# Performance work log

Measured on AMD Instinct MI355X. Metric: run time of the kernel, lower is better.

## Reference

```python
import jax, jax.numpy as jnp
import numpy as np
from jax import lax

HEADS = 8

def rotate_every_two(x):
    x1 = x[..., ::2]
    x2 = x[..., 1::2]
    return jnp.stack([-x2, x1], axis=-1).reshape(x.shape)

def theta_shift(x, sin, cos):
    # x: (b,n,N,d); sin/cos: (N,d) broadcast over b,n
    return x * cos + rotate_every_two(x) * sin

def setup_inputs() -> dict:
    key = jax.random.key(0)
    ks = jax.random.split(key, 8)
    B, C, H, W = 8, 256, 64, 64
    hd = C // HEADS
    return {
        'x': jax.random.normal(ks[0], (B, C, H, W), jnp.float32),
        'sin': jax.random.normal(ks[1], (H * W, hd), jnp.float32),
        'cos': jax.random.normal(ks[2], (H * W, hd), jnp.float32),
        'w_qkvo': jax.random.normal(ks[3], (4 * C, C), jnp.float32) * 0.02,
        'b_qkvo': jnp.zeros((4 * C,), jnp.float32),
        'w_lepe': jax.random.normal(ks[4], (C, 1, 5, 5), jnp.float32) * 0.02,
        'b_lepe': jnp.zeros((C,), jnp.float32),
        'w_proj': jax.random.normal(ks[5], (C, C), jnp.float32) * 0.02,
        'b_proj': jnp.zeros((C,), jnp.float32),
    }

def reference(x, sin, cos, w_qkvo, b_qkvo, w_lepe, b_lepe, w_proj, b_proj):
    B, C, H, W = x.shape
    heads = HEADS
    hd = C // heads
    N = H * W
    scale = hd ** (-0.5)

    # 1x1 conv qkvo
    qkvo = jnp.einsum('bchw,oc->bohw', x, w_qkvo) + b_qkvo[None, :, None, None]
    qkv = qkvo[:, :3 * C]
    o = qkvo[:, 3 * C:]

    # depthwise 5x5 lepe on v channels
    v_img = qkv[:, 2 * C:]
    lepe = lax.conv_general_dilated(
        v_img, w_lepe, (1, 1), [(2, 2), (2, 2)],
        dimension_numbers=('NCHW', 'OIHW', 'NCHW'),
        feature_group_count=C) + b_lepe[None, :, None, None]

    # b (m n d) h w -> m b n (h w) d
    qkv_r = qkv.reshape(B, 3, heads, hd, N).transpose(1, 0, 2, 4, 3)
    q, k, v = qkv_r[0], qkv_r[1], qkv_r[2]  # (b,n,N,d)

    q = jax.nn.elu(q) + 1.0
    k = jax.nn.elu(k) + 1.0

    # z = q @ mean_k^T * scale -> (b,n,N,1)
    z = jnp.einsum('bnld,bnd->bnl', q, k.mean(axis=2))[..., None] * scale

    q = theta_shift(q, sin, cos)
    k = theta_shift(k, sin, cos)

    s = (scale / N) ** 0.5
    kv = jnp.einsum('bnld,bnle->bnde', k * s, v * s)  # (b,n,d,d)
    v_mean = v.mean(axis=2, keepdims=True)  # (b,n,1,d)

    res = jnp.einsum('bnld,bnde->bnle', q, kv) * (1.0 + 1.0 / (z + 1e-6)) - z * v_mean

    # b n (h w) d -> b (n d) h w
    res = res.transpose(0, 1, 3, 2).reshape(B, C, H, W)
    res = res + lepe

    out = jnp.einsum('bchw,oc->bohw', res * o, w_proj) + b_proj[None, :, None, None]
    return out
```

## Files before the change

### kernel.cpp

```cpp
#include <hip/hip_runtime.h>
#include <hip/hip_bf16.h>

typedef unsigned short u16;
typedef unsigned int u32;
typedef short bf16x8 __attribute__((ext_vector_type(8)));
typedef float f32x4 __attribute__((ext_vector_type(4)));
typedef u32 u32x4 __attribute__((ext_vector_type(4)));

#define N_TOK 4096
#define C_DIM 256
#define HEADS 8
#define HD 32
#define SCALE_F 0.17677669529663687f

__device__ inline u16 f2bf(float f) {
    u32 u = __float_as_uint(f);
    u += 0x7fffu + ((u >> 16) & 1u);
    return (u16)(u >> 16);
}
__device__ inline float b2f(u16 h) { return __uint_as_float((u32)h << 16); }
__device__ inline float bf_lo(u32 u) { return __uint_as_float(u << 16); }
__device__ inline float bf_hi(u32 u) { return __uint_as_float(u & 0xffff0000u); }

__device__ inline void gload16(const void* g, void* l) {
    __builtin_amdgcn_global_load_lds((const __attribute__((address_space(1))) u32*)g,
                                     (__attribute__((address_space(3))) u32*)l, 16, 0, 0);
}

__global__ __launch_bounds__(256) void stage1(const float* __restrict__ x, const float* __restrict__ w1,
                                              const float* __restrict__ w2, const float* __restrict__ s,
                                              const float* __restrict__ c, u16* __restrict__ xT,
                                              u16* __restrict__ o1, u16* __restrict__ o2, u32* __restrict__ scT) {
    __shared__ char smem[16896];
    int bx = blockIdx.x;
    int t = threadIdx.x;
    if (bx < 2048) {
        int lt = bx & 63, ct = (bx >> 6) & 3, b = bx >> 8;
        int l0 = lt * 64, c0 = ct * 64;
        const float* xb = x + ((size_t)b * C_DIM + c0) * N_TOK + l0;
        float* tl = (float*)smem;
#pragma unroll
        for (int i = 0; i < 4; ++i) {
            int id = i * 256 + t;
            int ci = id >> 4, lj = id & 15;
            f32x4 v = *(const f32x4*)(xb + (size_t)ci * N_TOK + lj * 4);
#pragma unroll
            for (int e = 0; e < 4; ++e) tl[(lj * 4 + e) * 65 + ci] = v[e];
        }
        __syncthreads();
#pragma unroll
        for (int j = 0; j < 2; ++j) {
            int id = j * 256 + t;
            int l = id >> 3, cg = id & 7;
            u16 o[8];
#pragma unroll
            for (int e = 0; e < 8; ++e) o[e] = f2bf(tl[l * 65 + cg * 8 + e]);
            uint4 u;
            u.x = (u32)o[0] | ((u32)o[1] << 16);
            u.y = (u32)o[2] | ((u32)o[3] << 16);
            u.z = (u32)o[4] | ((u32)o[5] << 16);
            u.w = (u32)o[6] | ((u32)o[7] << 16);
            *(uint4*)(xT + ((size_t)b * N_TOK + l0 + l) * C_DIM + c0 + cg * 8) = u;
        }
        return;
    }
    int px = bx - 2048;
    if (px < 1024) {
        int i = px * 256 + t;
        o1[i] = f2bf(w1[i]);
        if (i < 256 * 256) o2[i] = f2bf(w2[i]);
        return;
    }
    int l0 = (px - 1024) * 64;
    float (*ts)[33] = (float(*)[33])smem;
    float (*tc)[33] = (float(*)[33])(smem + 8448);
    int d = t & 31, r = t >> 5;
#pragma unroll
    for (int i = 0; i < 8; ++i) {
        ts[r + i * 8][d] = s[(size_t)(l0 + r + i * 8) * HD + d];
        tc[r + i * 8][d] = c[(size_t)(l0 + r + i * 8) * HD + d];
    }
    __syncthreads();
    int li = t & 63, dr = t >> 6;
#pragma unroll
    for (int i = 0; i < 8; ++i) {
        int dd = dr * 8 + i;
        scT[(size_t)dd * N_TOK + l0 + li] = (u32)f2bf(ts[li][dd]) | ((u32)f2bf(tc[li][dd]) << 16);
    }
}

template <typename TO>
__global__ __launch_bounds__(256) void gemm_bt(const u16* __restrict__ A, const u16* __restrict__ Bm,
                                               const float* __restrict__ bias, TO* __restrict__ C,
                                               int M, int L, int K) {
    int bt = blockIdx.z;
    int m0 = blockIdx.y * 128;
    int l0 = blockIdx.x * 128;
    const u16* Bb = Bm + (size_t)bt * L * K;
    TO* Cb = C + (size_t)bt * M * L;

    __shared__ u16 smem[17408];
    u16* As = smem;
    u16* Bs = smem + 8192;
    u16* Cs = smem;

    int t = threadIdx.x;
    int w = t >> 6, lane = t & 63;
    int wr = (w >> 1) * 64, wc = (w & 1) * 64;
    int fr = lane & 15, kg = lane >> 4;

    f32x4 acc[4][4] = {};

    for (int k0 = 0; k0 < K; k0 += 64) {
#pragma unroll
        for (int j = 0; j < 4; ++j) {
            int c = j * 256 + w * 64 + lane;
            int row = c >> 3, slot = c & 7;
            int gslot = slot ^ (row & 7);
            u16* abase = As + (size_t)(j * 256 + w * 64) * 8;
            u16* bbase = Bs + (size_t)(j * 256 + w * 64) * 8;
            gload16(A + (size_t)(m0 + row) * K + k0 + gslot * 8, abase);
            gload16(Bb + (size_t)(l0 + row) * K + k0 + gslot * 8, bbase);
        }
        __syncthreads();
#pragma unroll
        for (int kk = 0; kk < 2; ++kk) {
            bf16x8 af[4], bfr[4];
#pragma unroll
            for (int i = 0; i < 4; ++i) {
                int ra = wr + i * 16 + fr;
                int rb = wc + i * 16 + fr;
                af[i]  = *(const bf16x8*)(As + (size_t)ra * 64 + (size_t)((kk * 4 + kg) ^ (ra & 7)) * 8);
                bfr[i] = *(const bf16x8*)(Bs + (size_t)rb * 64 + (size_t)((kk * 4 + kg) ^ (rb & 7)) * 8);
            }
#pragma unroll
            for (int i = 0; i < 4; ++i)
#pragma unroll
                for (int jj = 0; jj < 4; ++jj)
                    acc[i][jj] = __builtin_amdgcn_mfma_f32_16x16x32_bf16(af[i], bfr[jj], acc[i][jj], 0, 0, 0);
        }
        __syncthreads();
    }

    int rg = (lane >> 4) * 4;
    if constexpr (sizeof(TO) == 2) {
#pragma unroll
        for (int i = 0; i < 4; ++i)
#pragma unroll
            for (int jj = 0; jj < 4; ++jj) {
                int col = wc + jj * 16 + fr;
#pragma unroll
                for (int r = 0; r < 4; ++r) {
                    int row = wr + i * 16 + rg + r;
                    Cs[row * 136 + col] = f2bf(acc[i][jj][r] + bias[m0 + row]);
                }
            }
        __syncthreads();
        u16* CbT = (u16*)Cb;
#pragma unroll
        for (int j = 0; j < 8; ++j) {
            int id = j * 256 + t;
            int row = id >> 4, c8 = (id & 15) * 8;
            *(uint4*)(CbT + (size_t)(m0 + row) * L + l0 + c8) = *(const uint4*)(Cs + row * 136 + c8);
        }
    } else {
        float* Csf = (float*)smem;
#pragma unroll
        for (int half = 0; half < 2; ++half) {
            if ((w >> 1) == half) {
#pragma unroll
                for (int i = 0; i < 4; ++i)
#pragma unroll
                    for (int jj = 0; jj < 4; ++jj) {
                        int col = wc + jj * 16 + fr;
#pragma unroll
                        for (int r = 0; r < 4; ++r) {
                            int row = i * 16 + rg + r;
                            Csf[row * 132 + col] = acc[i][jj][r] + bias[m0 + half * 64 + row];
                        }
                    }
            }
            __syncthreads();
#pragma unroll
            for (int j = 0; j < 8; ++j) {
                int id = j * 256 + t;
                int row = id >> 5, c4 = id & 31;
                *(f32x4*)((float*)Cb + (size_t)(m0 + half * 64 + row) * L + l0 + c4 * 4) =
                    *(const f32x4*)(Csf + row * 132 + c4 * 4);
            }
            __syncthreads();
        }
    }
}

__global__ __launch_bounds__(256) void stage2(const u16* __restrict__ qkv, const u32* __restrict__ scT,
                                              const float* __restrict__ wl, const float* __restrict__ bl,
                                              float* __restrict__ part_kv, float* __restrict__ part_ks,
                                              float* __restrict__ part_vs, u16* __restrict__ lepe) {
    __shared__ char smem[34048];
    int bx = blockIdx.x;
    int t = threadIdx.x;

    if (bx >= 1024) {
        int i2 = bx - 1024;
        int c = i2 & 255, b = i2 >> 8;
        const u16* src = qkv + ((size_t)b * 512 + 256 + c) * N_TOK;
        u16* dst = lepe + ((size_t)b * C_DIM + c) * N_TOK;
        float* wc5 = (float*)smem;
        if (t < 25) wc5[t] = wl[c * 25 + t];
        __syncthreads();

        int h = t >> 2, w0 = (t & 3) * 16;
        float bb = bl[c];
        float o16[16];
#pragma unroll
        for (int i = 0; i < 16; ++i) o16[i] = bb;

#pragma unroll
        for (int dh = 0; dh < 5; ++dh) {
            int gr = h + dh - 2;
            bool rowok = (gr >= 0) && (gr < 64);
            const u16* rp = src + (size_t)(rowok ? gr : 0) * 64 + w0 - 8;
            bf16x8 L0 = ((const bf16x8*)rp)[0];
            bf16x8 L1 = ((const bf16x8*)rp)[1];
            bf16x8 L2 = ((const bf16x8*)rp)[2];
            bf16x8 L3 = ((const bf16x8*)rp)[3];
            float rbuf[32];
#pragma unroll
            for (int j = 0; j < 32; ++j) {
                int col = w0 - 8 + j;
                u16 raw = (u16)(j < 8 ? L0[j] : j < 16 ? L1[j - 8] : j < 24 ? L2[j - 16] : L3[j - 24]);
                bool ok = rowok && (col >= 0) && (col < 64);
                rbuf[j] = ok ? b2f(raw) : 0.f;
            }
#pragma unroll
            for (int dw = 0; dw < 5; ++dw) {
                float wv_ = wc5[dh * 5 + dw];
#pragma unroll
                for (int ow = 0; ow < 16; ++ow)
                    o16[ow] += rbuf[6 + dw + ow] * wv_;
            }
        }

        uint4 u0, u1;
        u0.x = (u32)f2bf(o16[0]) | ((u32)f2bf(o16[1]) << 16);
        u0.y = (u32)f2bf(o16[2]) | ((u32)f2bf(o16[3]) << 16);
        u0.z = (u32)f2bf(o16[4]) | ((u32)f2bf(o16[5]) << 16);
        u0.w = (u32)f2bf(o16[6]) | ((u32)f2bf(o16[7]) << 16);
        u1.x = (u32)f2bf(o16[8]) | ((u32)f2bf(o16[9]) << 16);
        u1.y = (u32)f2bf(o16[10]) | ((u32)f2bf(o16[11]) << 16);
        u1.z = (u32)f2bf(o16[12]) | ((u32)f2bf(o16[13]) << 16);
        u1.w = (u32)f2bf(o16[14]) | ((u32)f2bf(o16[15]) << 16);
        *(uint4*)(dst + h * 64 + w0) = u0;
        *(uint4*)(dst + h * 64 + w0 + 8) = u1;
        return;
    }

    int chunk = bx & 15, bn = bx >> 4;
    int b = bn >> 3, n = bn & 7;
    const u16* kp = qkv + ((size_t)b * 512 + n * HD) * N_TOK;
    const u16* vp = qkv + ((size_t)b * 512 + 256 + n * HD) * N_TOK;
    int lbase = chunk * 256;

    u16 (*ks_bf)[136] = (u16(*)[136])smem;
    u16 (*v_bf)[136]  = (u16(*)[136])(smem + 8704);
    float* red  = (float*)(smem + 17408);
    float* redk = (float*)(smem + 33792);
    float* redv = (float*)(smem + 33920);

    int w = t >> 6, lane = t & 63;
    int fr = lane & 15, kg = lane >> 4;
    int p = t >> 4, g = t & 15;
    int dv = t >> 3, g2 = t & 7;

    f32x4 acc[2][2] = {};
    float ks0 = 0.f, ks1 = 0.f, vs = 0.f;

    for (int st = 0; st < 2; ++st) {
        int tok0 = lbase + st * 128;
        if (st) __syncthreads();
        const u16* k0p = kp + (size_t)(2 * p) * N_TOK + tok0 + g * 8;
        const u16* k1p = k0p + N_TOK;
        const u32* s0p = scT + (size_t)(2 * p) * N_TOK + tok0 + g * 8;
        const u32* s1p = s0p + N_TOK;
        bf16x8 k0 = *(const bf16x8*)k0p;
        bf16x8 k1 = *(const bf16x8*)k1p;
        u32x4 s0a = ((const u32x4*)s0p)[0], s0b = ((const u32x4*)s0p)[1];
        u32x4 s1a = ((const u32x4*)s1p)[0], s1b = ((const u32x4*)s1p)[1];
        const u16* vpp = vp + (size_t)dv * N_TOK + tok0 + g2 * 16;
        bf16x8 va = ((const bf16x8*)vpp)[0];
        bf16x8 vb = ((const bf16x8*)vpp)[1];

        u16 o0[8], o1[8];
#pragma unroll
        for (int j = 0; j < 8; ++j) {
            float kv0 = b2f((u16)k0[j]);
            float kv1 = b2f((u16)k1[j]);
            u32 sc0 = j < 4 ? s0a[j] : s0b[j - 4];
            u32 sc1 = j < 4 ? s1a[j] : s1b[j - 4];
            float e0 = kv0 > 0.f ? kv0 + 1.f : __expf(kv0);
            float e1 = kv1 > 0.f ? kv1 + 1.f : __expf(kv1);
            ks0 += e0; ks1 += e1;
            float se = bf_lo(sc0), ce = bf_hi(sc0);
            float so = bf_lo(sc1), co = bf_hi(sc1);
            o0[j] = f2bf(e0 * ce - e1 * se);
            o1[j] = f2bf(e1 * co + e0 * so);
        }
        u32x4 w0, w1;
#pragma unroll
        for (int q = 0; q < 4; ++q) {
            w0[q] = (u32)o0[2 * q] | ((u32)o0[2 * q + 1] << 16);
            w1[q] = (u32)o1[2 * q] | ((u32)o1[2 * q + 1] << 16);
        }
        *(u32x4*)&ks_bf[2 * p][g * 8] = w0;
        *(u32x4*)&ks_bf[2 * p + 1][g * 8] = w1;

#pragma unroll
        for (int j = 0; j < 8; ++j) { vs += b2f((u16)va[j]); }
#pragma unroll
        for (int j = 0; j < 8; ++j) { vs += b2f((u16)vb[j]); }
        *(bf16x8*)&v_bf[dv][g2 * 16] = va;
        *(bf16x8*)&v_bf[dv][g2 * 16 + 8] = vb;
        __syncthreads();

        int kcol = w * 32 + kg * 8;
        bf16x8 af[2], bfv[2];
#pragma unroll
        for (int i = 0; i < 2; ++i) {
            af[i]  = *(const bf16x8*)&ks_bf[i * 16 + fr][kcol];
            bfv[i] = *(const bf16x8*)&v_bf[i * 16 + fr][kcol];
        }
#pragma unroll
        for (int i = 0; i < 2; ++i)
#pragma unroll
            for (int jj = 0; jj < 2; ++jj)
                acc[i][jj] = __builtin_amdgcn_mfma_f32_16x16x32_bf16(af[i], bfv[jj], acc[i][jj], 0, 0, 0);
    }

#pragma unroll
    for (int i = 0; i < 2; ++i)
#pragma unroll
        for (int jj = 0; jj < 2; ++jj)
#pragma unroll
            for (int r = 0; r < 4; ++r) {
                int row = i * 16 + kg * 4 + r;
                int col = jj * 16 + fr;
                red[w * 1024 + row * 32 + col] = acc[i][jj][r];
            }

#pragma unroll
    for (int m = 1; m < 16; m <<= 1) {
        ks0 += __shfl_xor(ks0, m);
        ks1 += __shfl_xor(ks1, m);
    }
    if ((lane & 15) == 0) { redk[2 * p] = ks0; redk[2 * p + 1] = ks1; }
#pragma unroll
    for (int m = 1; m < 8; m <<= 1) vs += __shfl_xor(vs, m);
    if ((lane & 7) == 0) redv[dv] = vs;
    __syncthreads();

    float* pkv = part_kv + ((size_t)bn * 16 + chunk) * 1024;
#pragma unroll
    for (int i = 0; i < 4; ++i) {
        int el = i * 256 + t;
        pkv[el] = red[el] + red[1024 + el] + red[2048 + el] + red[3072 + el];
    }
    if (t < 32) {
        part_ks[((size_t)bn * 16 + chunk) * 32 + t] = redk[t];
        part_vs[((size_t)bn * 16 + chunk) * 32 + t] = redv[t];
    }
}

__global__ __launch_bounds__(256) void kv_final(const float* __restrict__ part_kv, const float* __restrict__ part_ks,
                                                const float* __restrict__ part_vs, u16* __restrict__ kvT_bf,
                                                float* __restrict__ kmean, float* __restrict__ vmean) {
    int bn = blockIdx.x;
    int t = threadIdx.x;
    const float* p = part_kv + (size_t)bn * 16 * 1024;
    const float s2c = SCALE_F / (float)N_TOK;
#pragma unroll
    for (int i = 0; i < 4; ++i) {
        int sl = t + i * 256;
        float s = 0;
#pragma unroll
        for (int c = 0; c < 16; ++c) s += p[(size_t)c * 1024 + sl];
        float val = s * s2c;
        int d = sl >> 5, e = sl & 31;
        kvT_bf[(size_t)bn * 1024 + e * 32 + d] = f2bf(val);
    }
    if (t < 32) {
        float s = 0, sv = 0;
        for (int c = 0; c < 16; ++c) {
            s  += part_ks[((size_t)bn * 16 + c) * 32 + t];
            sv += part_vs[((size_t)bn * 16 + c) * 32 + t];
        }
        kmean[bn * 32 + t] = s * (1.f / (float)N_TOK);
        vmean[bn * 32 + t] = sv * (1.f / (float)N_TOK);
    }
}

__global__ __launch_bounds__(256) void attn_epilogue(const u16* __restrict__ wbf, const float* __restrict__ bq,
                                                     const u16* __restrict__ xT, const u32* __restrict__ scT,
                                                     const u16* __restrict__ kvT_bf, const float* __restrict__ kmean,
                                                     const float* __restrict__ vmean, const u16* __restrict__ lepe,
                                                     u16* __restrict__ resnT) {
    int lt = blockIdx.x, bn = blockIdx.y;
    int b = bn >> 3, n = bn & 7;
    int T0 = lt * 256;
    const u16* lp = lepe + ((size_t)b * C_DIM + n * HD) * N_TOK;
    const u16* Bx = xT + ((size_t)b * N_TOK + T0) * C_DIM;

    __shared__ char smem[64256];
    u16* qA    = (u16*)smem;
    u16* o_lds = (u16*)(smem + 20480);
    u16* Rt    = (u16*)(smem + 40960);
    u16* kvb   = (u16*)(smem + 61440);
    float* kml = (float*)(smem + 64000);
    float* vml = (float*)(smem + 64128);
    u16* Bst = (u16*)smem;
    u16* Ast = (u16*)(smem + 32768);

    int t = threadIdx.x;
    int w = t >> 6, lane = t & 63;
    int fr = lane & 15, kg = lane >> 4;

    if (t < 128) {
        int e = t >> 2, d0 = (t & 3) * 8;
        *(uint4*)(kvb + e * 40 + d0) = *(const uint4*)(kvT_bf + (size_t)bn * 1024 + e * 32 + d0);
    }
    if (t < 32) { kml[t] = kmean[bn * 32 + t]; vml[t] = vmean[bn * 32 + t]; }

    f32x4 acc[4][4] = {};
    for (int k0 = 0; k0 < 256; k0 += 64) {
#pragma unroll
        for (int j = 0; j < 8; ++j) {
            int c = j * 256 + w * 64 + lane;
            int row = c >> 3, slot = c & 7;
            int gslot = slot ^ (row & 7);
            gload16(Bx + (size_t)row * C_DIM + k0 + gslot * 8, Bst + (size_t)(j * 256 + w * 64) * 8);
        }
#pragma unroll
        for (int j = 0; j < 2; ++j) {
            int c = j * 256 + w * 64 + lane;
            int row = c >> 3, slot = c & 7;
            int gslot = slot ^ (row & 7);
            int arow = (row < 32 ? n * HD : 736 + n * HD) + row;
            gload16(wbf + (size_t)arow * C_DIM + k0 + gslot * 8, Ast + (size_t)(j * 256 + w * 64) * 8);
        }
        __syncthreads();
#pragma unroll
        for (int kk = 0; kk < 2; ++kk) {
            bf16x8 af[4], bfr[4];
#pragma unroll
            for (int i = 0; i < 4; ++i) {
                int ra = i * 16 + fr;
                af[i] = *(const bf16x8*)(Ast + (size_t)ra * 64 + (size_t)((kk * 4 + kg) ^ (ra & 7)) * 8);
            }
#pragma unroll
            for (int jj = 0; jj < 4; ++jj) {
                int rb = w * 64 + jj * 16 + fr;
                bfr[jj] = *(const bf16x8*)(Bst + (size_t)rb * 64 + (size_t)((kk * 4 + kg) ^ (rb & 7)) * 8);
            }
#pragma unroll
            for (int i = 0; i < 4; ++i)
#pragma unroll
                for (int jj = 0; jj < 4; ++jj)
                    acc[i][jj] = __builtin_amdgcn_mfma_f32_16x16x32_bf16(af[i], bfr[jj], acc[i][jj], 0, 0, 0);
        }
        __syncthreads();
    }
    int rg = kg * 4;
#pragma unroll
    for (int i = 0; i < 4; ++i)
#pragma unroll
        for (int jj = 0; jj < 4; ++jj) {
            int tok = w * 64 + jj * 16 + fr;
#pragma unroll
            for (int r = 0; r < 4; ++r) {
                int qorow = i * 16 + rg + r;
                int brow = (qorow < 32 ? n * HD : 736 + n * HD) + qorow;
                u16 val = f2bf(acc[i][jj][r] + bq[brow]);
                if (qorow < 32) qA[tok * 40 + qorow] = val;
                else            o_lds[tok * 40 + qorow - 32] = val;
            }
        }
    __syncthreads();

    int token = T0 + t;
    float qv[32];
    float z = 0.f;
#pragma unroll
    for (int j = 0; j < 4; ++j) {
        bf16x8 q8 = *(const bf16x8*)(qA + t * 40 + j * 8);
#pragma unroll
        for (int e = 0; e < 8; ++e) {
            float x_ = b2f((u16)q8[e]);
            float e_ = x_ > 0.f ? x_ + 1.f : __expf(x_);
            qv[j * 8 + e] = e_;
            z += e_ * kml[j * 8 + e];
        }
    }
    z *= SCALE_F;
#pragma unroll
    for (int p = 0; p < 16; ++p) {
        u32 sc0 = scT[(size_t)(2 * p) * N_TOK + token];
        u32 sc1 = scT[(size_t)(2 * p + 1) * N_TOK + token];
        float se = bf_lo(sc0), ce = bf_hi(sc0);
        float so = bf_lo(sc1), co = bf_hi(sc1);
        float a = qv[2 * p], bb = qv[2 * p + 1];
        qv[2 * p]     = a * ce - bb * se;
        qv[2 * p + 1] = bb * co + a * so;
    }
    float mult = 1.f + 1.f / (z + 1e-6f);
#pragma unroll
    for (int j4 = 0; j4 < 4; ++j4) {
        uint4 u;
        u.x = (u32)f2bf(qv[8 * j4 + 0]) | ((u32)f2bf(qv[8 * j4 + 1]) << 16);
        u.y = (u32)f2bf(qv[8 * j4 + 2]) | ((u32)f2bf(qv[8 * j4 + 3]) << 16);
        u.z = (u32)f2bf(qv[8 * j4 + 4]) | ((u32)f2bf(qv[8 * j4 + 5]) << 16);
        u.w = (u32)f2bf(qv[8 * j4 + 6]) | ((u32)f2bf(qv[8 * j4 + 7]) << 16);
        *(uint4*)(qA + t * 40 + j4 * 8) = u;
    }
    __syncthreads();

    {
        bf16x8 af[4], bfr[2];
#pragma unroll
        for (int i = 0; i < 4; ++i)
            af[i] = *(const bf16x8*)(qA + (size_t)(w * 64 + i * 16 + fr) * 40 + kg * 8);
#pragma unroll
        for (int jj = 0; jj < 2; ++jj)
            bfr[jj] = *(const bf16x8*)(kvb + (jj * 16 + fr) * 40 + kg * 8);

        u16* Rw = Rt + w * 2560;
        f32x4 zero = {0.f, 0.f, 0.f, 0.f};
#pragma unroll
        for (int i = 0; i < 4; ++i)
#pragma unroll
            for (int jj = 0; jj < 2; ++jj) {
                f32x4 a2 = __builtin_amdgcn_mfma_f32_16x16x32_bf16(af[i], bfr[jj], zero, 0, 0, 0);
#pragma unroll
                for (int r = 0; r < 4; ++r)
                    Rw[(i * 16 + kg * 4 + r) * 40 + jj * 16 + fr] = f2bf(a2[r]);
            }
    }
    __syncthreads();

    float res[32], ovv[32];
#pragma unroll
    for (int j = 0; j < 4; ++j) {
        bf16x8 r8 = *(const bf16x8*)(Rt + w * 2560 + lane * 40 + j * 8);
        bf16x8 o8 = *(const bf16x8*)(o_lds + t * 40 + j * 8);
#pragma unroll
        for (int e = 0; e < 8; ++e) {
            res[j * 8 + e] = b2f((u16)r8[e]);
            ovv[j * 8 + e] = b2f((u16)o8[e]);
        }
    }

    u16* dst0 = resnT + ((size_t)b * N_TOK + token) * C_DIM + n * HD;
#pragma unroll
    for (int g = 0; g < 4; ++g) {
        float vv[8];
#pragma unroll
        for (int e2 = 0; e2 < 8; ++e2) {
            int ee = g * 8 + e2;
            float lx = b2f(lp[(size_t)ee * N_TOK + token]);
            float rx = res[ee] * mult - z * vml[ee];
            vv[e2] = (rx + lx) * ovv[ee];
        }
        uint4 u;
        u.x = (u32)f2bf(vv[0]) | ((u32)f2bf(vv[1]) << 16);
        u.y = (u32)f2bf(vv[2]) | ((u32)f2bf(vv[3]) << 16);
        u.z = (u32)f2bf(vv[4]) | ((u32)f2bf(vv[5]) << 16);
        u.w = (u32)f2bf(vv[6]) | ((u32)f2bf(vv[7]) << 16);
        ((uint4*)(dst0 + g * 8))[0] = u;
    }
}

extern "C" void kernel_launch(void* const* d_in, const int* in_sizes, int n_in,
                              void* d_out, int out_size, void* d_ws, size_t ws_size,
                              hipStream_t stream) {
    const float* x      = (const float*)d_in[0];
    const float* sinp   = (const float*)d_in[1];
    const float* cosp   = (const float*)d_in[2];
    const float* w_qkvo = (const float*)d_in[3];
    const float* b_qkvo = (const float*)d_in[4];
    const float* w_lepe = (const float*)d_in[5];
    const float* b_lepe = (const float*)d_in[6];
    const float* w_proj = (const float*)d_in[7];
    const float* b_proj = (const float*)d_in[8];

    char* ws = (char*)d_ws;
    size_t off = 0;
    auto alloc = [&](size_t bytes) { size_t o = off; off = (off + bytes + 255) & ~(size_t)255; return o; };
    u16*   wbf     = (u16*)(ws + alloc((size_t)1024 * 256 * 2));
    u16*   wpbf    = (u16*)(ws + alloc((size_t)256 * 256 * 2));
    u16*   xT      = (u16*)(ws + alloc((size_t)8 * 4096 * 256 * 2));
    u16*   qkv     = (u16*)(ws + alloc((size_t)8 * 512 * 4096 * 2));
    u16*   lepe    = (u16*)(ws + alloc((size_t)8 * 256 * 4096 * 2));
    u16*   resnT   = (u16*)(ws + alloc((size_t)8 * 4096 * 256 * 2));
    float* part_kv = (float*)(ws + alloc((size_t)64 * 16 * 1024 * 4));
    float* part_ks = (float*)(ws + alloc((size_t)64 * 16 * 32 * 4));
    float* part_vs = (float*)(ws + alloc((size_t)64 * 16 * 32 * 4));
    u16*   kvT_bf  = (u16*)(ws + alloc((size_t)64 * 1024 * 2));
    float* kmean   = (float*)(ws + alloc((size_t)64 * 32 * 4));
    float* vmean   = (float*)(ws + alloc((size_t)64 * 32 * 4));
    u32*   scT     = (u32*)(ws + alloc((size_t)32 * 4096 * 4));
    if (off > ws_size) return;

    stage1<<<dim3(3136), dim3(256), 0, stream>>>(x, w_qkvo, w_proj, sinp, cosp, xT, wbf, wpbf, scT);
    gemm_bt<u16><<<dim3(32, 4, 8), dim3(256), 0, stream>>>(wbf + 256 * 256, xT, b_qkvo + 256, qkv, 512, 4096, 256);
    stage2<<<dim3(3072), dim3(256), 0, stream>>>(qkv, scT, w_lepe, b_lepe, part_kv, part_ks, part_vs, lepe);
    kv_final<<<dim3(64), dim3(256), 0, stream>>>(part_kv, part_ks, part_vs, kvT_bf, kmean, vmean);
    attn_epilogue<<<dim3(16, 64), dim3(256), 0, stream>>>(wbf, b_qkvo, xT, scT, kvT_bf, kmean, vmean, lepe, resnT);
    gemm_bt<float><<<dim3(32, 2, 8), dim3(256), 0, stream>>>(wpbf, resnT, b_proj, (float*)d_out, 256, 4096, 256);
}
```

Before: 94.98 us.

## Fuse K/V projection GEMM into KV-reduction kernel and merge lepe with kv_final

The separate K/V projection GEMM, which wrote a full bf16 K and V tensor to global memory, is removed. Each stage2_kv block now computes its K and V tile for one head and one 256-token chunk with MFMA, applies ELU and the rotary shift in registers, and accumulates the partial kv and the k and v sums. Only V is written back, because the depthwise lepe convolution still needs it. The lepe convolution moves out of stage2 and is merged with kv_final into a single launch. This saves one kernel launch and the K round-trip to memory, but the GEMM now uses a 64x256 tile per block and the x tile is reloaded once for each of the 8 heads.

```diff
diff --git a/kernel.cpp b/kernel.cpp
--- a/kernel.cpp
+++ b/kernel.cpp
@@ -89,20 +89,18 @@
     }
 }
 
-template <typename TO>
-__global__ __launch_bounds__(256) void gemm_bt(const u16* __restrict__ A, const u16* __restrict__ Bm,
-                                               const float* __restrict__ bias, TO* __restrict__ C,
-                                               int M, int L, int K) {
+__global__ __launch_bounds__(256) void gemm_proj(const u16* __restrict__ A, const u16* __restrict__ Bm,
+                                                 const float* __restrict__ bias, float* __restrict__ C,
+                                                 int M, int L, int K) {
     int bt = blockIdx.z;
     int m0 = blockIdx.y * 128;
     int l0 = blockIdx.x * 128;
     const u16* Bb = Bm + (size_t)bt * L * K;
-    TO* Cb = C + (size_t)bt * M * L;
+    float* Cb = C + (size_t)bt * M * L;
 
     __shared__ u16 smem[17408];
     u16* As = smem;
     u16* Bs = smem + 8192;
-    u16* Cs = smem;
 
     int t = threadIdx.x;
     int w = t >> 6, lane = t & 63;
@@ -143,187 +141,166 @@
     }
 
     int rg = (lane >> 4) * 4;
-    if constexpr (sizeof(TO) == 2) {
-#pragma unroll
-        for (int i = 0; i < 4; ++i)
-#pragma unroll
-            for (int jj = 0; jj < 4; ++jj) {
-                int col = wc + jj * 16 + fr;
-#pragma unroll
-                for (int r = 0; r < 4; ++r) {
-                    int row = wr + i * 16 + rg + r;
-                    Cs[row * 136 + col] = f2bf(acc[i][jj][r] + bias[m0 + row]);
+    float* Csf = (float*)smem;
+#pragma unroll
+    for (int half = 0; half < 2; ++half) {
+        if ((w >> 1) == half) {
+#pragma unroll
+            for (int i = 0; i < 4; ++i)
+#pragma unroll
+                for (int jj = 0; jj < 4; ++jj) {
+                    int col = wc + jj * 16 + fr;
+#pragma unroll
+                    for (int r = 0; r < 4; ++r) {
+                        int row = i * 16 + rg + r;
+                        Csf[row * 132 + col] = acc[i][jj][r] + bias[m0 + half * 64 + row];
+                    }
                 }
-            }
-        __syncthreads();
-        u16* CbT = (u16*)Cb;
+        }
+        __syncthreads();
 #pragma unroll
         for (int j = 0; j < 8; ++j) {
             int id = j * 256 + t;
-            int row = id >> 4, c8 = (id & 15) * 8;
-            *(uint4*)(CbT + (size_t)(m0 + row) * L + l0 + c8) = *(const uint4*)(Cs + row * 136 + c8);
-        }
-    } else {
-        float* Csf = (float*)smem;
-#pragma unroll
-        for (int half = 0; half < 2; ++half) {
-            if ((w >> 1) == half) {
-#pragma unroll
-                for (int i = 0; i < 4; ++i)
-#pragma unroll
-                    for (int jj = 0; jj < 4; ++jj) {
-                        int col = wc + jj * 16 + fr;
-#pragma unroll
-                        for (int r = 0; r < 4; ++r) {
-                            int row = i * 16 + rg + r;
-                            Csf[row * 132 + col] = acc[i][jj][r] + bias[m0 + half * 64 + row];
-                        }
-                    }
-            }
-            __syncthreads();
-#pragma unroll
-            for (int j = 0; j < 8; ++j) {
-                int id = j * 256 + t;
-                int row = id >> 5, c4 = id & 31;
-                *(f32x4*)((float*)Cb + (size_t)(m0 + half * 64 + row) * L + l0 + c4 * 4) =
-                    *(const f32x4*)(Csf + row * 132 + c4 * 4);
-            }
-            __syncthreads();
-        }
-    }
-}
-
-__global__ __launch_bounds__(256) void stage2(const u16* __restrict__ qkv, const u32* __restrict__ scT,
-                                              const float* __restrict__ wl, const float* __restrict__ bl,
-                                              float* __restrict__ part_kv, float* __restrict__ part_ks,
-                                              float* __restrict__ part_vs, u16* __restrict__ lepe) {
-    __shared__ char smem[34048];
-    int bx = blockIdx.x;
+            int row = id >> 5, c4 = id & 31;
+            *(f32x4*)(Cb + (size_t)(m0 + half * 64 + row) * L + l0 + c4 * 4) =
+                *(const f32x4*)(Csf + row * 132 + c4 * 4);
+        }
+        __syncthreads();
+    }
+}
+
+__global__ __launch_bounds__(256) void stage2_kv(const u16* __restrict__ wbf, const float* __restrict__ bq,
+                                                 const u16* __restrict__ xT, const u32* __restrict__ scT,
+                                                 u16* __restrict__ v_glob, float* __restrict__ part_kv,
+                                                 float* __restrict__ part_ks, float* __restrict__ part_vs) {
+    int chunk = blockIdx.x & 15, bn = blockIdx.x >> 4;
+    int b = bn >> 3, n = bn & 7;
+    int T0 = chunk * 256;
+    const u16* Bx = xT + ((size_t)b * N_TOK + T0) * C_DIM;
+
+    __shared__ char smem[51200];
+    u16* Bst = (u16*)smem;
+    u16* Ast = (u16*)(smem + 32768);
+    u16 (*ks_bf)[264] = (u16(*)[264])smem;
+    u16 (*v_bf)[264]  = (u16(*)[264])(smem + 16896);
+    float* red  = (float*)(smem + 33792);
+    float* redk = (float*)(smem + 50176);
+    float* redv = (float*)(smem + 50688);
+
     int t = threadIdx.x;
-
-    if (bx >= 1024) {
-        int i2 = bx - 1024;
-        int c = i2 & 255, b = i2 >> 8;
-        const u16* src = qkv + ((size_t)b * 512 + 256 + c) * N_TOK;
-        u16* dst = lepe + ((size_t)b * C_DIM + c) * N_TOK;
-        float* wc5 = (float*)smem;
-        if (t < 25) wc5[t] = wl[c * 25 + t];
-        __syncthreads();
-
-        int h = t >> 2, w0 = (t & 3) * 16;
-        float bb = bl[c];
-        float o16[16];
-#pragma unroll
-        for (int i = 0; i < 16; ++i) o16[i] = bb;
-
-#pragma unroll
-        for (int dh = 0; dh < 5; ++dh) {
-            int gr = h + dh - 2;
-            bool rowok = (gr >= 0) && (gr < 64);
-            const u16* rp = src + (size_t)(rowok ? gr : 0) * 64 + w0 - 8;
-            bf16x8 L0 = ((const bf16x8*)rp)[0];
-            bf16x8 L1 = ((const bf16x8*)rp)[1];
-            bf16x8 L2 = ((const bf16x8*)rp)[2];
-            bf16x8 L3 = ((const bf16x8*)rp)[3];
-            float rbuf[32];
-#pragma unroll
-            for (int j = 0; j < 32; ++j) {
-                int col = w0 - 8 + j;
-                u16 raw = (u16)(j < 8 ? L0[j] : j < 16 ? L1[j - 8] : j < 24 ? L2[j - 16] : L3[j - 24]);
-                bool ok = rowok && (col >= 0) && (col < 64);
-                rbuf[j] = ok ? b2f(raw) : 0.f;
-            }
-#pragma unroll
-            for (int dw = 0; dw < 5; ++dw) {
-                float wv_ = wc5[dh * 5 + dw];
-#pragma unroll
-                for (int ow = 0; ow < 16; ++ow)
-                    o16[ow] += rbuf[6 + dw + ow] * wv_;
-            }
-        }
-
-        uint4 u0, u1;
-        u0.x = (u32)f2bf(o16[0]) | ((u32)f2bf(o16[1]) << 16);
-        u0.y = (u32)f2bf(o16[2]) | ((u32)f2bf(o16[3]) << 16);
-        u0.z = (u32)f2bf(o16[4]) | ((u32)f2bf(o16[5]) << 16);
-        u0.w = (u32)f2bf(o16[6]) | ((u32)f2bf(o16[7]) << 16);
-        u1.x = (u32)f2bf(o16[8]) | ((u32)f2bf(o16[9]) << 16);
-        u1.y = (u32)f2bf(o16[10]) | ((u32)f2bf(o16[11]) << 16);
-        u1.z = (u32)f2bf(o16[12]) | ((u32)f2bf(o16[13]) << 16);
-        u1.w = (u32)f2bf(o16[14]) | ((u32)f2bf(o16[15]) << 16);
-        *(uint4*)(dst + h * 64 + w0) = u0;
-        *(uint4*)(dst + h * 64 + w0 + 8) = u1;
-        return;
-    }
-
-    int chunk = bx & 15, bn = bx >> 4;
-    int b = bn >> 3, n = bn & 7;
-    const u16* kp = qkv + ((size_t)b * 512 + n * HD) * N_TOK;
-    const u16* vp = qkv + ((size_t)b * 512 + 256 + n * HD) * N_TOK;
-    int lbase = chunk * 256;
-
-    u16 (*ks_bf)[136] = (u16(*)[136])smem;
-    u16 (*v_bf)[136]  = (u16(*)[136])(smem + 8704);
-    float* red  = (float*)(smem + 17408);
-    float* redk = (float*)(smem + 33792);
-    float* redv = (float*)(smem + 33920);
-
     int w = t >> 6, lane = t & 63;
     int fr = lane & 15, kg = lane >> 4;
-    int p = t >> 4, g = t & 15;
-    int dv = t >> 3, g2 = t & 7;
-
-    f32x4 acc[2][2] = {};
-    float ks0 = 0.f, ks1 = 0.f, vs = 0.f;
-
-    for (int st = 0; st < 2; ++st) {
-        int tok0 = lbase + st * 128;
-        if (st) __syncthreads();
-        const u16* k0p = kp + (size_t)(2 * p) * N_TOK + tok0 + g * 8;
-        const u16* k1p = k0p + N_TOK;
-        const u32* s0p = scT + (size_t)(2 * p) * N_TOK + tok0 + g * 8;
-        const u32* s1p = s0p + N_TOK;
-        bf16x8 k0 = *(const bf16x8*)k0p;
-        bf16x8 k1 = *(const bf16x8*)k1p;
-        u32x4 s0a = ((const u32x4*)s0p)[0], s0b = ((const u32x4*)s0p)[1];
-        u32x4 s1a = ((const u32x4*)s1p)[0], s1b = ((const u32x4*)s1p)[1];
-        const u16* vpp = vp + (size_t)dv * N_TOK + tok0 + g2 * 16;
-        bf16x8 va = ((const bf16x8*)vpp)[0];
-        bf16x8 vb = ((const bf16x8*)vpp)[1];
-
-        u16 o0[8], o1[8];
+
+    float bk[8], bv[8];
+#pragma unroll
+    for (int i = 0; i < 2; ++i)
+#pragma unroll
+        for (int r = 0; r < 4; ++r) {
+            bk[i * 4 + r] = bq[256 + n * HD + i * 16 + kg * 4 + r];
+            bv[i * 4 + r] = bq[512 + n * HD + i * 16 + kg * 4 + r];
+        }
+
+    f32x4 acc[4][4] = {};
+    for (int k0 = 0; k0 < 256; k0 += 64) {
 #pragma unroll
         for (int j = 0; j < 8; ++j) {
-            float kv0 = b2f((u16)k0[j]);
-            float kv1 = b2f((u16)k1[j]);
-            u32 sc0 = j < 4 ? s0a[j] : s0b[j - 4];
-            u32 sc1 = j < 4 ? s1a[j] : s1b[j - 4];
-            float e0 = kv0 > 0.f ? kv0 + 1.f : __expf(kv0);
-            float e1 = kv1 > 0.f ? kv1 + 1.f : __expf(kv1);
-            ks0 += e0; ks1 += e1;
-            float se = bf_lo(sc0), ce = bf_hi(sc0);
-            float so = bf_lo(sc1), co = bf_hi(sc1);
-            o0[j] = f2bf(e0 * ce - e1 * se);
-            o1[j] = f2bf(e1 * co + e0 * so);
-        }
-        u32x4 w0, w1;
-#pragma unroll
-        for (int q = 0; q < 4; ++q) {
-            w0[q] = (u32)o0[2 * q] | ((u32)o0[2 * q + 1] << 16);
-            w1[q] = (u32)o1[2 * q] | ((u32)o1[2 * q + 1] << 16);
-        }
-        *(u32x4*)&ks_bf[2 * p][g * 8] = w0;
-        *(u32x4*)&ks_bf[2 * p + 1][g * 8] = w1;
-
-#pragma unroll
-        for (int j = 0; j < 8; ++j) { vs += b2f((u16)va[j]); }
-#pragma unroll
-        for (int j = 0; j < 8; ++j) { vs += b2f((u16)vb[j]); }
-        *(bf16x8*)&v_bf[dv][g2 * 16] = va;
-        *(bf16x8*)&v_bf[dv][g2 * 16 + 8] = vb;
-        __syncthreads();
-
-        int kcol = w * 32 + kg * 8;
+            int c = j * 256 + w * 64 + lane;
+            int row = c >> 3, slot = c & 7;
+            int gslot = slot ^ (row & 7);
+            gload16(Bx + (size_t)row * C_DIM + k0 + gslot * 8, Bst + (size_t)(j * 256 + w * 64) * 8);
+        }
+#pragma unroll
+        for (int j = 0; j < 2; ++j) {
+            int c = j * 256 + w * 64 + lane;
+            int row = c >> 3, slot = c & 7;
+            int gslot = slot ^ (row & 7);
+            int arow = (row < 32 ? 256 : 480) + n * HD + row;
+            gload16(wbf + (size_t)arow * C_DIM + k0 + gslot * 8, Ast + (size_t)(j * 256 + w * 64) * 8);
+        }
+        __syncthreads();
+#pragma unroll
+        for (int kk = 0; kk < 2; ++kk) {
+            bf16x8 af[4], bfr[4];
+#pragma unroll
+            for (int i = 0; i < 4; ++i) {
+                int ra = i * 16 + fr;
+                af[i] = *(const bf16x8*)(Ast + (size_t)ra * 64 + (size_t)((kk * 4 + kg) ^ (ra & 7)) * 8);
+            }
+#pragma unroll
+            for (int jj = 0; jj < 4; ++jj) {
+                int rb = w * 64 + jj * 16 + fr;
+                bfr[jj] = *(const bf16x8*)(Bst + (size_t)rb * 64 + (size_t)((kk * 4 + kg) ^ (rb & 7)) * 8);
+            }
+#pragma unroll
+            for (int i = 0; i < 4; ++i)
+#pragma unroll
+                for (int jj = 0; jj < 4; ++jj)
+                    acc[i][jj] = __builtin_amdgcn_mfma_f32_16x16x32_bf16(af[i], bfr[jj], acc[i][jj], 0, 0, 0);
+        }
+        __syncthreads();
+    }
+
+    float kspart[8] = {}, vspart[8] = {};
+#pragma unroll
+    for (int i = 0; i < 2; ++i)
+#pragma unroll
+        for (int jj = 0; jj < 4; ++jj) {
+            int tok = w * 64 + jj * 16 + fr;
+            float k0v = acc[i][jj][0] + bk[i * 4 + 0];
+            float k1v = acc[i][jj][1] + bk[i * 4 + 1];
+            float k2v = acc[i][jj][2] + bk[i * 4 + 2];
+            float k3v = acc[i][jj][3] + bk[i * 4 + 3];
+            float e0 = k0v > 0.f ? k0v + 1.f : __expf(k0v);
+            float e1 = k1v > 0.f ? k1v + 1.f : __expf(k1v);
+            float e2 = k2v > 0.f ? k2v + 1.f : __expf(k2v);
+            float e3 = k3v > 0.f ? k3v + 1.f : __expf(k3v);
+            kspart[i * 4 + 0] += e0; kspart[i * 4 + 1] += e1;
+            kspart[i * 4 + 2] += e2; kspart[i * 4 + 3] += e3;
+            int d0 = i * 16 + kg * 4;
+            u32 sA = scT[(size_t)(d0 + 0) * N_TOK + T0 + tok];
+            u32 sB = scT[(size_t)(d0 + 1) * N_TOK + T0 + tok];
+            u32 sC = scT[(size_t)(d0 + 2) * N_TOK + T0 + tok];
+            u32 sD = scT[(size_t)(d0 + 3) * N_TOK + T0 + tok];
+            ks_bf[d0 + 0][tok] = f2bf(e0 * bf_hi(sA) - e1 * bf_lo(sA));
+            ks_bf[d0 + 1][tok] = f2bf(e1 * bf_hi(sB) + e0 * bf_lo(sB));
+            ks_bf[d0 + 2][tok] = f2bf(e2 * bf_hi(sC) - e3 * bf_lo(sC));
+            ks_bf[d0 + 3][tok] = f2bf(e3 * bf_hi(sD) + e2 * bf_lo(sD));
+        }
+#pragma unroll
+    for (int i = 2; i < 4; ++i)
+#pragma unroll
+        for (int jj = 0; jj < 4; ++jj) {
+            int tok = w * 64 + jj * 16 + fr;
+#pragma unroll
+            for (int r = 0; r < 4; ++r) {
+                int vrow = (i - 2) * 16 + kg * 4 + r;
+                float vv_ = acc[i][jj][r] + bv[(i - 2) * 4 + r];
+                vspart[(i - 2) * 4 + r] += vv_;
+                v_bf[vrow][tok] = f2bf(vv_);
+            }
+        }
+#pragma unroll
+    for (int m = 1; m < 16; m <<= 1) {
+#pragma unroll
+        for (int q = 0; q < 8; ++q) {
+            kspart[q] += __shfl_xor(kspart[q], m);
+            vspart[q] += __shfl_xor(vspart[q], m);
+        }
+    }
+    if (fr == 0) {
+#pragma unroll
+        for (int q = 0; q < 8; ++q) {
+            int row = (q >> 2) * 16 + kg * 4 + (q & 3);
+            redk[w * 32 + row] = kspart[q];
+            redv[w * 32 + row] = vspart[q];
+        }
+    }
+    __syncthreads();
+
+    f32x4 a2[2][2] = {};
+#pragma unroll
+    for (int kc = 0; kc < 2; ++kc) {
+        int kcol = w * 64 + kc * 32 + kg * 8;
         bf16x8 af[2], bfv[2];
 #pragma unroll
         for (int i = 0; i < 2; ++i) {
@@ -334,7 +311,21 @@
         for (int i = 0; i < 2; ++i)
 #pragma unroll
             for (int jj = 0; jj < 2; ++jj)
-                acc[i][jj] = __builtin_amdgcn_mfma_f32_16x16x32_bf16(af[i], bfv[jj], acc[i][jj], 0, 0, 0);
+                a2[i][jj] = __builtin_amdgcn_mfma_f32_16x16x32_bf16(af[i], bfv[jj], a2[i][jj], 0, 0, 0);
+    }
+
+    {
+        int row = t >> 3, tg = t & 7;
+        u16* vg = v_glob + ((size_t)(b * C_DIM + n * HD + row)) * N_TOK + T0 + tg * 32;
+#pragma unroll
+        for (int q = 0; q < 4; ++q)
+            *(uint4*)(vg + q * 8) = *(const uint4*)&v_bf[row][tg * 32 + q * 8];
+    }
+    if (t < 32) {
+        float s = redk[t] + redk[32 + t] + redk[64 + t] + redk[96 + t];
+        float sv = redv[t] + redv[32 + t] + redv[64 + t] + redv[96 + t];
+        part_ks[((size_t)bn * 16 + chunk) * 32 + t] = s;
+        part_vs[((size_t)bn * 16 + chunk) * 32 + t] = sv;
     }
 
 #pragma unroll
@@ -345,58 +336,100 @@
             for (int r = 0; r < 4; ++r) {
                 int row = i * 16 + kg * 4 + r;
                 int col = jj * 16 + fr;
-                red[w * 1024 + row * 32 + col] = acc[i][jj][r];
-            }
-
-#pragma unroll
-    for (int m = 1; m < 16; m <<= 1) {
-        ks0 += __shfl_xor(ks0, m);
-        ks1 += __shfl_xor(ks1, m);
-    }
-    if ((lane & 15) == 0) { redk[2 * p] = ks0; redk[2 * p + 1] = ks1; }
-#pragma unroll
-    for (int m = 1; m < 8; m <<= 1) vs += __shfl_xor(vs, m);
-    if ((lane & 7) == 0) redv[dv] = vs;
+                red[w * 1024 + row * 32 + col] = a2[i][jj][r];
+            }
     __syncthreads();
-
     float* pkv = part_kv + ((size_t)bn * 16 + chunk) * 1024;
 #pragma unroll
     for (int i = 0; i < 4; ++i) {
         int el = i * 256 + t;
         pkv[el] = red[el] + red[1024 + el] + red[2048 + el] + red[3072 + el];
     }
-    if (t < 32) {
-        part_ks[((size_t)bn * 16 + chunk) * 32 + t] = redk[t];
-        part_vs[((size_t)bn * 16 + chunk) * 32 + t] = redv[t];
-    }
-}
-
-__global__ __launch_bounds__(256) void kv_final(const float* __restrict__ part_kv, const float* __restrict__ part_ks,
-                                                const float* __restrict__ part_vs, u16* __restrict__ kvT_bf,
-                                                float* __restrict__ kmean, float* __restrict__ vmean) {
-    int bn = blockIdx.x;
+}
+
+__global__ __launch_bounds__(256) void kvfinal_lepe(const float* __restrict__ part_kv, const float* __restrict__ part_ks,
+                                                    const float* __restrict__ part_vs, const u16* __restrict__ v_glob,
+                                                    const float* __restrict__ wl, const float* __restrict__ bl,
+                                                    u16* __restrict__ kvT_bf, float* __restrict__ kmean,
+                                                    float* __restrict__ vmean, u16* __restrict__ lepe) {
+    __shared__ float wc5[25];
+    int bx = blockIdx.x;
     int t = threadIdx.x;
-    const float* p = part_kv + (size_t)bn * 16 * 1024;
-    const float s2c = SCALE_F / (float)N_TOK;
-#pragma unroll
-    for (int i = 0; i < 4; ++i) {
-        int sl = t + i * 256;
-        float s = 0;
-#pragma unroll
-        for (int c = 0; c < 16; ++c) s += p[(size_t)c * 1024 + sl];
-        float val = s * s2c;
-        int d = sl >> 5, e = sl & 31;
-        kvT_bf[(size_t)bn * 1024 + e * 32 + d] = f2bf(val);
-    }
-    if (t < 32) {
-        float s = 0, sv = 0;
-        for (int c = 0; c < 16; ++c) {
-            s  += part_ks[((size_t)bn * 16 + c) * 32 + t];
-            sv += part_vs[((size_t)bn * 16 + c) * 32 + t];
-        }
-        kmean[bn * 32 + t] = s * (1.f / (float)N_TOK);
-        vmean[bn * 32 + t] = sv * (1.f / (float)N_TOK);
-    }
+    if (bx < 64) {
+        int bn = bx;
+        const float* p = part_kv + (size_t)bn * 16 * 1024;
+        const float s2c = SCALE_F / (float)N_TOK;
+#pragma unroll
+        for (int i = 0; i < 4; ++i) {
+            int sl = t + i * 256;
+            float s = 0;
+#pragma unroll
+            for (int c = 0; c < 16; ++c) s += p[(size_t)c * 1024 + sl];
+            float val = s * s2c;
+            int d = sl >> 5, e = sl & 31;
+            kvT_bf[(size_t)bn * 1024 + e * 32 + d] = f2bf(val);
+        }
+        if (t < 32) {
+            float s = 0, sv = 0;
+            for (int c = 0; c < 16; ++c) {
+                s  += part_ks[((size_t)bn * 16 + c) * 32 + t];
+                sv += part_vs[((size_t)bn * 16 + c) * 32 + t];
+            }
+            kmean[bn * 32 + t] = s * (1.f / (float)N_TOK);
+            vmean[bn * 32 + t] = sv * (1.f / (float)N_TOK);
+        }
+        return;
+    }
+    int i2 = bx - 64;
+    int c = i2 & 255, b = i2 >> 8;
+    const u16* src = v_glob + ((size_t)(b * C_DIM + c)) * N_TOK;
+    u16* dst = lepe + ((size_t)b * C_DIM + c) * N_TOK;
+    if (t < 25) wc5[t] = wl[c * 25 + t];
+    __syncthreads();
+
+    int h = t >> 2, w0 = (t & 3) * 16;
+    float bb = bl[c];
+    float o16[16];
+#pragma unroll
+    for (int i = 0; i < 16; ++i) o16[i] = bb;
+
+#pragma unroll
+    for (int dh = 0; dh < 5; ++dh) {
+        int gr = h + dh - 2;
+        bool rowok = (gr >= 0) && (gr < 64);
+        const u16* rp = src + (size_t)(rowok ? gr : 0) * 64 + w0 - 8;
+        bf16x8 L0 = ((const bf16x8*)rp)[0];
+        bf16x8 L1 = ((const bf16x8*)rp)[1];
+        bf16x8 L2 = ((const bf16x8*)rp)[2];
+        bf16x8 L3 = ((const bf16x8*)rp)[3];
+        float rbuf[32];
+#pragma unroll
+        for (int j = 0; j < 32; ++j) {
+            int col = w0 - 8 + j;
+            u16 raw = (u16)(j < 8 ? L0[j] : j < 16 ? L1[j - 8] : j < 24 ? L2[j - 16] : L3[j - 24]);
+            bool ok = rowok && (col >= 0) && (col < 64);
+            rbuf[j] = ok ? b2f(raw) : 0.f;
+        }
+#pragma unroll
+        for (int dw = 0; dw < 5; ++dw) {
+            float wv_ = wc5[dh * 5 + dw];
+#pragma unroll
+            for (int ow = 0; ow < 16; ++ow)
+                o16[ow] += rbuf[6 + dw + ow] * wv_;
+        }
+    }
+
+    uint4 u0, u1;
+    u0.x = (u32)f2bf(o16[0]) | ((u32)f2bf(o16[1]) << 16);
+    u0.y = (u32)f2bf(o16[2]) | ((u32)f2bf(o16[3]) << 16);
+    u0.z = (u32)f2bf(o16[4]) | ((u32)f2bf(o16[5]) << 16);
+    u0.w = (u32)f2bf(o16[6]) | ((u32)f2bf(o16[7]) << 16);
+    u1.x = (u32)f2bf(o16[8]) | ((u32)f2bf(o16[9]) << 16);
+    u1.y = (u32)f2bf(o16[10]) | ((u32)f2bf(o16[11]) << 16);
+    u1.z = (u32)f2bf(o16[12]) | ((u32)f2bf(o16[13]) << 16);
+    u1.w = (u32)f2bf(o16[14]) | ((u32)f2bf(o16[15]) << 16);
+    *(uint4*)(dst + h * 64 + w0) = u0;
+    *(uint4*)(dst + h * 64 + w0 + 8) = u1;
 }
 
 __global__ __launch_bounds__(256) void attn_epilogue(const u16* __restrict__ wbf, const float* __restrict__ bq,
@@ -597,7 +630,7 @@
     u16*   wbf     = (u16*)(ws + alloc((size_t)1024 * 256 * 2));
     u16*   wpbf    = (u16*)(ws + alloc((size_t)256 * 256 * 2));
     u16*   xT      = (u16*)(ws + alloc((size_t)8 * 4096 * 256 * 2));
-    u16*   qkv     = (u16*)(ws + alloc((size_t)8 * 512 * 4096 * 2));
+    u16*   v_glob  = (u16*)(ws + alloc((size_t)8 * 256 * 4096 * 2));
     u16*   lepe    = (u16*)(ws + alloc((size_t)8 * 256 * 4096 * 2));
     u16*   resnT   = (u16*)(ws + alloc((size_t)8 * 4096 * 256 * 2));
     float* part_kv = (float*)(ws + alloc((size_t)64 * 16 * 1024 * 4));
@@ -610,9 +643,9 @@
     if (off > ws_size) return;
 
     stage1<<<dim3(3136), dim3(256), 0, stream>>>(x, w_qkvo, w_proj, sinp, cosp, xT, wbf, wpbf, scT);
-    gemm_bt<u16><<<dim3(32, 4, 8), dim3(256), 0, stream>>>(wbf + 256 * 256, xT, b_qkvo + 256, qkv, 512, 4096, 256);
-    stage2<<<dim3(3072), dim3(256), 0, stream>>>(qkv, scT, w_lepe, b_lepe, part_kv, part_ks, part_vs, lepe);
-    kv_final<<<dim3(64), dim3(256), 0, stream>>>(part_kv, part_ks, part_vs, kvT_bf, kmean, vmean);
+    stage2_kv<<<dim3(1024), dim3(256), 0, stream>>>(wbf, b_qkvo, xT, scT, v_glob, part_kv, part_ks, part_vs);
+    kvfinal_lepe<<<dim3(2112), dim3(256), 0, stream>>>(part_kv, part_ks, part_vs, v_glob, w_lepe, b_lepe,
+                                                       kvT_bf, kmean, vmean, lepe);
     attn_epilogue<<<dim3(16, 64), dim3(256), 0, stream>>>(wbf, b_qkvo, xT, scT, kvT_bf, kmean, vmean, lepe, resnT);
-    gemm_bt<float><<<dim3(32, 2, 8), dim3(256), 0, stream>>>(wpbf, resnT, b_proj, (float*)d_out, 256, 4096, 256);
-}
+    gemm_proj<<<dim3(32, 2, 8), dim3(256), 0, stream>>>(wpbf, resnT, b_proj, (float*)d_out, 256, 4096, 256);
+}
```

Result: faster. 92.75 us (-2.3%).
